# Kernel tuning notes

Hardware: AMD Instinct MI355X
Metric: run time of the kernel (lower is better)

## Reference

```python
import jax, jax.numpy as jnp
import numpy as np

B, NQ, NK, D = 8, 4096, 4096, 512


def setup_inputs() -> dict:
    key = jax.random.key(0)
    ks = jax.random.split(key, 8)
    s = 1.0 / np.sqrt(D)
    return {
        "x": jax.random.normal(ks[0], (B, NQ, D), dtype=jnp.float32),
        "context": jax.random.normal(ks[1], (B, NK, D), dtype=jnp.float32),
        "Wq": jax.random.normal(ks[2], (D, D), dtype=jnp.float32) * s,
        "bq": jax.random.normal(ks[3], (D,), dtype=jnp.float32) * 0.01,
        "Wk": jax.random.normal(ks[4], (D, D), dtype=jnp.float32) * s,
        "bk": jax.random.normal(ks[5], (D,), dtype=jnp.float32) * 0.01,
        "Wv": jax.random.normal(ks[6], (D, D), dtype=jnp.float32) * s,
        "bv": jax.random.normal(ks[7], (D,), dtype=jnp.float32) * 0.01,
    }


def reference(x, context, Wq, bq, Wk, bk, Wv, bv):
    # torch Linear: y = x @ W.T + b, W is [out, in]
    Q = jnp.einsum('bnd,ed->bne', x, Wq) + bq          # [B, NQ, D]
    K = jnp.einsum('bmd,ed->bme', context, Wk) + bk    # [B, NK, D]
    V = jnp.einsum('bmd,ed->bme', context, Wv) + bv    # [B, NK, D]
    scale = 1.0 / jnp.sqrt(jnp.asarray(x.shape[-1], dtype=x.dtype))
    scores = jnp.einsum('bne,bme->bnm', Q, K) * scale  # [B, NQ, NK]
    attn = jax.nn.softmax(scores, axis=-1)
    return jnp.einsum('bnm,bme->bne', attn, V)         # [B, NQ, D]
```

## Files before the change

### kernel.cpp

```cpp
#include <hip/hip_runtime.h>
#include <math.h>

typedef unsigned short u16;
typedef unsigned int u32;
typedef __attribute__((ext_vector_type(8))) short short8;
typedef __attribute__((ext_vector_type(4))) float floatx4;

#define DEVINL static __device__ __forceinline__

DEVINL u32 pk2(float a, float b) {
  u32 r;
  asm("v_cvt_pk_bf16_f32 %0, %1, %2" : "=v"(r) : "v"(a), "v"(b));
  return r;
}
DEVINL float exp2fast(float x) {
  float r;
  asm("v_exp_f32 %0, %1" : "=v"(r) : "v"(x));
  return r;
}

DEVINL void gload16(const void* g, void* lds_base) {
  __builtin_amdgcn_global_load_lds(
      (const __attribute__((address_space(1))) void*)g,
      (__attribute__((address_space(3))) void*)lds_base, 16, 0, 0);
}

DEVINL void stage_a_f32(const float* __restrict__ A, int lda, int gm0, int k0,
                        u16* As, int tid) {
  const int idx = tid & 127;
  const int row8 = idx >> 4;
  const int k16h = idx & 15;
  const int chsel = tid >> 7;
#pragma unroll
  for (int rr = 0; rr < 8; ++rr) {
    const int chunk = rr * 2 + chsel;
    const float4 v = *(const float4*)(A + (long)(gm0 + chunk * 8 + row8) * lda + k0 + k16h * 4);
    const int baddr = chunk * 1024 + row8 * 128 + (((k16h >> 1) ^ row8) << 4) + ((k16h & 1) << 3);
    uint2 p; p.x = pk2(v.x, v.y); p.y = pk2(v.z, v.w);
    *(uint2*)((char*)As + baddr) = p;
  }
}

__global__ __launch_bounds__(256) void cast4_kernel(const float* __restrict__ in,
                                                    u16* __restrict__ out, long n4) {
  long i = (long)blockIdx.x * blockDim.x + threadIdx.x;
  long stride = (long)gridDim.x * blockDim.x;
  for (; i < n4; i += stride) {
    float4 v = ((const float4*)in)[i];
    uint2 o; o.x = pk2(v.x, v.y); o.y = pk2(v.z, v.w);
    ((uint2*)out)[i] = o;
  }
}

__global__ __launch_bounds__(256) void zerof(float* __restrict__ p, int n4) {
  int i = blockIdx.x * 256 + threadIdx.x;
  if (i < n4) ((float4*)p)[i] = make_float4(0.f, 0.f, 0.f, 0.f);
}

__global__ __launch_bounds__(256) void proj_q(const float* __restrict__ A,
                                              const u16* __restrict__ Bt,
                                              const float* __restrict__ bias,
                                              u16* __restrict__ C, float oscale) {
  __shared__ u16 As[8192];
  __shared__ u16 Bs[8192];
  const int tid = threadIdx.x;
  const int lane = tid & 63;
  const int wave = tid >> 6;
  const int gm0 = blockIdx.y * 128;
  const int gn0 = blockIdx.x * 128;
  const int wm = (wave >> 1) * 64;
  const int wn = (wave & 1) * 64;

  floatx4 acc[4][4];
#pragma unroll
  for (int i = 0; i < 4; ++i)
#pragma unroll
    for (int j = 0; j < 4; ++j)
#pragma unroll
      for (int r = 0; r < 4; ++r) acc[i][j][r] = 0.0f;

  const int lrow = lane >> 3;
  const int lcol = (lane & 7) ^ lrow;
  const int fr_row = lane & 15;
  const int fr_k16 = lane >> 4;

  for (int k0 = 0; k0 < 512; k0 += 64) {
#pragma unroll
    for (int c = 0; c < 4; ++c) {
      const int ch = wave * 4 + c;
      gload16(Bt + (long)(gn0 + ch * 8 + lrow) * 512 + k0 + lcol * 8, (char*)Bs + ch * 1024);
    }
    stage_a_f32(A, 512, gm0, k0, As, tid);
    __syncthreads();
#pragma unroll
    for (int ks = 0; ks < 2; ++ks) {
      const int c16 = ks * 4 + fr_k16;
      short8 af[4], bfv[4];
#pragma unroll
      for (int i = 0; i < 4; ++i) {
        const int m = wm + i * 16 + fr_row;
        const int slot = (m >> 3) * 64 + (m & 7) * 8 + (c16 ^ (m & 7));
        af[i] = *(const short8*)((const char*)As + slot * 16);
      }
#pragma unroll
      for (int j = 0; j < 4; ++j) {
        const int n = wn + j * 16 + fr_row;
        const int slot = (n >> 3) * 64 + (n & 7) * 8 + (c16 ^ (n & 7));
        bfv[j] = *(const short8*)((const char*)Bs + slot * 16);
      }
#pragma unroll
      for (int i = 0; i < 4; ++i)
#pragma unroll
        for (int j = 0; j < 4; ++j)
          acc[i][j] = __builtin_amdgcn_mfma_f32_16x16x32_bf16(af[i], bfv[j], acc[i][j], 0, 0, 0);
    }
    __syncthreads();
  }

  const int crow = (lane >> 4) * 4;
  const int ccol = lane & 15;
#pragma unroll
  for (int i = 0; i < 4; ++i)
#pragma unroll
    for (int j = 0; j < 4; ++j) {
      const int n = gn0 + wn + j * 16 + ccol;
      const float badd = bias[n];
      const float a0 = (acc[i][j][0] + badd) * oscale;
      const float a1 = (acc[i][j][1] + badd) * oscale;
      const float a2 = (acc[i][j][2] + badd) * oscale;
      const float a3 = (acc[i][j][3] + badd) * oscale;
      const u32 p01 = pk2(a0, a1);
      const u32 p23 = pk2(a2, a3);
      u16* cp = C + (long)(gm0 + wm + i * 16 + crow) * 512 + n;
      cp[0]    = (u16)p01;
      cp[512]  = (u16)(p01 >> 16);
      cp[1024] = (u16)p23;
      cp[1536] = (u16)(p23 >> 16);
    }
}

__global__ __launch_bounds__(256) void proj_kv(const float* __restrict__ A,
                                               const u16* __restrict__ Wk,
                                               const float* __restrict__ bk,
                                               const u16* __restrict__ Wv,
                                               const float* __restrict__ bv,
                                               u16* __restrict__ Kb,
                                               u16* __restrict__ Vt) {
  __shared__ u16 As[8192];
  __shared__ u16 Bs[8192];
  const int tid = threadIdx.x;
  const int lane = tid & 63;
  const int wave = tid >> 6;
  const int isV = blockIdx.x >> 2;
  const u16* Bt = isV ? Wv : Wk;
  const float* bias = isV ? bv : bk;
  const int gm0 = blockIdx.y * 128;
  const int gn0 = (blockIdx.x & 3) * 128;
  const int wm = (wave >> 1) * 64;
  const int wn = (wave & 1) * 64;

  floatx4 acc[4][4];
#pragma unroll
  for (int i = 0; i < 4; ++i)
#pragma unroll
    for (int j = 0; j < 4; ++j)
#pragma unroll
      for (int r = 0; r < 4; ++r) acc[i][j][r] = 0.0f;

  const int lrow = lane >> 3;
  const int lcol = (lane & 7) ^ lrow;
  const int fr_row = lane & 15;
  const int fr_k16 = lane >> 4;

  for (int k0 = 0; k0 < 512; k0 += 64) {
#pragma unroll
    for (int c = 0; c < 4; ++c) {
      const int ch = wave * 4 + c;
      gload16(Bt + (long)(gn0 + ch * 8 + lrow) * 512 + k0 + lcol * 8, (char*)Bs + ch * 1024);
    }
    stage_a_f32(A, 512, gm0, k0, As, tid);
    __syncthreads();
#pragma unroll
    for (int ks = 0; ks < 2; ++ks) {
      const int c16 = ks * 4 + fr_k16;
      short8 af[4], bfv[4];
#pragma unroll
      for (int i = 0; i < 4; ++i) {
        const int m = wm + i * 16 + fr_row;
        const int slot = (m >> 3) * 64 + (m & 7) * 8 + (c16 ^ (m & 7));
        af[i] = *(const short8*)((const char*)As + slot * 16);
      }
#pragma unroll
      for (int j = 0; j < 4; ++j) {
        const int n = wn + j * 16 + fr_row;
        const int slot = (n >> 3) * 64 + (n & 7) * 8 + (c16 ^ (n & 7));
        bfv[j] = *(const short8*)((const char*)Bs + slot * 16);
      }
#pragma unroll
      for (int i = 0; i < 4; ++i)
#pragma unroll
        for (int j = 0; j < 4; ++j)
          acc[i][j] = __builtin_amdgcn_mfma_f32_16x16x32_bf16(af[i], bfv[j], acc[i][j], 0, 0, 0);
    }
    __syncthreads();
  }

  const int crow = (lane >> 4) * 4;
  const int ccol = lane & 15;
  if (!isV) {
#pragma unroll
    for (int i = 0; i < 4; ++i)
#pragma unroll
      for (int j = 0; j < 4; ++j) {
        const int n = gn0 + wn + j * 16 + ccol;
        const float badd = bias[n];
        const u32 p01 = pk2(acc[i][j][0] + badd, acc[i][j][1] + badd);
        const u32 p23 = pk2(acc[i][j][2] + badd, acc[i][j][3] + badd);
        u16* cp = Kb + (long)(gm0 + wm + i * 16 + crow) * 512 + n;
        cp[0]    = (u16)p01;
        cp[512]  = (u16)(p01 >> 16);
        cp[1024] = (u16)p23;
        cp[1536] = (u16)(p23 >> 16);
      }
  } else {
#pragma unroll
    for (int i = 0; i < 4; ++i)
#pragma unroll
      for (int j = 0; j < 4; ++j) {
        const int n = gn0 + wn + j * 16 + ccol;
        const float badd = bias[n];
        const int m = gm0 + wm + i * 16 + crow;
        const int b = m >> 12;
        const int mm = m & 4095;
        uint2 st;
        st.x = pk2(acc[i][j][0] + badd, acc[i][j][1] + badd);
        st.y = pk2(acc[i][j][2] + badd, acc[i][j][3] + badd);
        *(uint2*)(Vt + (long)b * 512 * 4096 + (long)n * 4096 + mm) = st;
      }
  }
}

__global__ __launch_bounds__(256) void gemm_s(
    const u16* __restrict__ A, const u16* __restrict__ Bt, u16* __restrict__ S,
    float* __restrict__ Ld, long aBS, long bBS) {
  __shared__ u16 As[8192];
  __shared__ u16 Bs[8192];
  const int tid = threadIdx.x;
  const int lane = tid & 63;
  const int wave = tid >> 6;
  const int bz = blockIdx.z;
  A += (long)bz * aBS;
  Bt += (long)bz * bBS;
  u16* Sb = S + (long)bz * 4096 * 4096;
  const int gm0 = blockIdx.y * 128;
  const int gn0 = blockIdx.x * 128;
  const int wm = (wave >> 1) * 64;
  const int wn = (wave & 1) * 64;

  floatx4 acc[4][4];
#pragma unroll
  for (int i = 0; i < 4; ++i)
#pragma unroll
    for (int j = 0; j < 4; ++j)
#pragma unroll
      for (int r = 0; r < 4; ++r) acc[i][j][r] = 0.0f;

  const int lrow = lane >> 3;
  const int lcol = (lane & 7) ^ lrow;
  const int fr_row = lane & 15;
  const int fr_k16 = lane >> 4;

  for (int k0 = 0; k0 < 512; k0 += 64) {
#pragma unroll
    for (int c = 0; c < 4; ++c) {
      const int ch = wave * 4 + c;
      const int r = ch * 8 + lrow;
      gload16(A + (long)(gm0 + r) * 512 + k0 + lcol * 8, (char*)As + ch * 1024);
      gload16(Bt + (long)(gn0 + r) * 512 + k0 + lcol * 8, (char*)Bs + ch * 1024);
    }
    __syncthreads();
#pragma unroll
    for (int ks = 0; ks < 2; ++ks) {
      const int c16 = ks * 4 + fr_k16;
      short8 af[4], bfv[4];
#pragma unroll
      for (int i = 0; i < 4; ++i) {
        const int m = wm + i * 16 + fr_row;
        const int slot = (m >> 3) * 64 + (m & 7) * 8 + (c16 ^ (m & 7));
        af[i] = *(const short8*)((const char*)As + slot * 16);
      }
#pragma unroll
      for (int j = 0; j < 4; ++j) {
        const int n = wn + j * 16 + fr_row;
        const int slot = (n >> 3) * 64 + (n & 7) * 8 + (c16 ^ (n & 7));
        bfv[j] = *(const short8*)((const char*)Bs + slot * 16);
      }
#pragma unroll
      for (int i = 0; i < 4; ++i)
#pragma unroll
        for (int j = 0; j < 4; ++j)
          acc[i][j] = __builtin_amdgcn_mfma_f32_16x16x32_bf16(af[i], bfv[j], acc[i][j], 0, 0, 0);
    }
    __syncthreads();
  }

  const int crow = (lane >> 4) * 4;
  const int ccol = lane & 15;
  float (*sml)[2] = (float (*)[2])As;
#pragma unroll
  for (int i = 0; i < 4; ++i) {
    float rs0 = 0.f, rs1 = 0.f, rs2 = 0.f, rs3 = 0.f;
    u16* sp = Sb + (long)(gm0 + wm + i * 16 + crow) * 4096 + gn0 + wn + ccol;
#pragma unroll
    for (int j = 0; j < 4; ++j) {
      const float e0 = exp2fast(acc[i][j][0]);
      const float e1 = exp2fast(acc[i][j][1]);
      const float e2 = exp2fast(acc[i][j][2]);
      const float e3 = exp2fast(acc[i][j][3]);
      const u32 p01 = pk2(e0, e1);
      const u32 p23 = pk2(e2, e3);
      u16* q = sp + j * 16;
      q[0]     = (u16)p01;
      q[4096]  = (u16)(p01 >> 16);
      q[8192]  = (u16)p23;
      q[12288] = (u16)(p23 >> 16);
      rs0 += e0; rs1 += e1; rs2 += e2; rs3 += e3;
    }
#pragma unroll
    for (int off = 1; off < 16; off <<= 1) {
      rs0 += __shfl_xor(rs0, off, 64);
      rs1 += __shfl_xor(rs1, off, 64);
      rs2 += __shfl_xor(rs2, off, 64);
      rs3 += __shfl_xor(rs3, off, 64);
    }
    if ((lane & 15) == 0) {
      const int rb = wm + i * 16 + crow;
      sml[rb + 0][wave & 1] = rs0;
      sml[rb + 1][wave & 1] = rs1;
      sml[rb + 2][wave & 1] = rs2;
      sml[rb + 3][wave & 1] = rs3;
    }
  }
  __syncthreads();
  if (tid < 128)
    atomicAdd(&Ld[(long)bz * 4096 + gm0 + tid], sml[tid][0] + sml[tid][1]);
}

__global__ __launch_bounds__(256) void gemm_o(
    const u16* __restrict__ A, const u16* __restrict__ Bt, float* __restrict__ Cout,
    const float* __restrict__ Ld, long aBS, long bBS, long cBS) {
  __shared__ u16 As[4096];
  __shared__ u16 Bs[8192];
  const int tid = threadIdx.x;
  const int lane = tid & 63;
  const int wave = tid >> 6;
  const int bz = blockIdx.z;
  A += (long)bz * aBS;
  Bt += (long)bz * bBS;
  const long cbase = (long)bz * cBS;
  const int gm0 = blockIdx.y * 64;
  const int gn0 = blockIdx.x * 128;
  const int wn = wave * 32;

  floatx4 acc[4][2];
#pragma unroll
  for (int i = 0; i < 4; ++i)
#pragma unroll
    for (int j = 0; j < 2; ++j)
#pragma unroll
      for (int r = 0; r < 4; ++r) acc[i][j][r] = 0.0f;

  const int lrow = lane >> 3;
  const int lcol = (lane & 7) ^ lrow;
  const int fr_row = lane & 15;
  const int fr_k16 = lane >> 4;

  for (int k0 = 0; k0 < 4096; k0 += 64) {
#pragma unroll
    for (int c = 0; c < 2; ++c) {
      const int ch = wave * 2 + c;
      gload16(A + (long)(gm0 + ch * 8 + lrow) * 4096 + k0 + lcol * 8, (char*)As + ch * 1024);
    }
#pragma unroll
    for (int c = 0; c < 4; ++c) {
      const int ch = wave * 4 + c;
      gload16(Bt + (long)(gn0 + ch * 8 + lrow) * 4096 + k0 + lcol * 8, (char*)Bs + ch * 1024);
    }
    __syncthreads();
#pragma unroll
    for (int ks = 0; ks < 2; ++ks) {
      const int c16 = ks * 4 + fr_k16;
      short8 af[4], bfv[2];
#pragma unroll
      for (int i = 0; i < 4; ++i) {
        const int m = i * 16 + fr_row;
        const int slot = (m >> 3) * 64 + (m & 7) * 8 + (c16 ^ (m & 7));
        af[i] = *(const short8*)((const char*)As + slot * 16);
      }
#pragma unroll
      for (int j = 0; j < 2; ++j) {
        const int n = wn + j * 16 + fr_row;
        const int slot = (n >> 3) * 64 + (n & 7) * 8 + (c16 ^ (n & 7));
        bfv[j] = *(const short8*)((const char*)Bs + slot * 16);
      }
#pragma unroll
      for (int i = 0; i < 4; ++i)
#pragma unroll
        for (int j = 0; j < 2; ++j)
          acc[i][j] = __builtin_amdgcn_mfma_f32_16x16x32_bf16(af[i], bfv[j], acc[i][j], 0, 0, 0);
    }
    __syncthreads();
  }

  const int crow = (lane >> 4) * 4;
  const int ccol = lane & 15;
  float linv[4][4];
#pragma unroll
  for (int i = 0; i < 4; ++i)
#pragma unroll
    for (int r = 0; r < 4; ++r)
      linv[i][r] = 1.0f / Ld[(long)bz * 4096 + gm0 + i * 16 + crow + r];
#pragma unroll
  for (int i = 0; i < 4; ++i)
#pragma unroll
    for (int j = 0; j < 2; ++j) {
      const int n = gn0 + wn + j * 16 + ccol;
#pragma unroll
      for (int r = 0; r < 4; ++r) {
        const int m = gm0 + i * 16 + crow + r;
        Cout[cbase + (long)m * 512 + n] = acc[i][j][r] * linv[i][r];
      }
    }
}

extern "C" void kernel_launch(void* const* d_in, const int* in_sizes, int n_in,
                              void* d_out, int out_size, void* d_ws, size_t ws_size,
                              hipStream_t stream) {
  const int B = 8, NQ = 4096, NK = 4096, D = 512;
  const long nX = (long)B * NQ * D;
  const long nW = (long)D * D;
  const float oscale = 0.044194173824159216f * 1.4426950408889634f;

  const float* x = (const float*)d_in[0];
  const float* ctx = (const float*)d_in[1];
  const float* Wq = (const float*)d_in[2];
  const float* bq = (const float*)d_in[3];
  const float* Wk = (const float*)d_in[4];
  const float* bk = (const float*)d_in[5];
  const float* Wv = (const float*)d_in[6];
  const float* bv = (const float*)d_in[7];
  float* out = (float*)d_out;

  size_t off = 0;
  auto alloc = [&](size_t bytes) { size_t o = off; off = (off + bytes + 255) & ~(size_t)255; return o; };
  char* ws = (char*)d_ws;
  u16* Qb  = (u16*)(ws + alloc(nX * 2));
  u16* Kb  = (u16*)(ws + alloc(nX * 2));
  u16* Vt  = (u16*)(ws + alloc(nX * 2));
  float* Ld = (float*)(ws + alloc((size_t)B * NQ * 4));
  const size_t s_off = off;
  u16* wqb = (u16*)(ws + alloc(nW * 2));
  u16* wkb = (u16*)(ws + alloc(nW * 2));
  u16* wvb = (u16*)(ws + alloc(nW * 2));
  u16* S   = (u16*)(ws + s_off);

  const size_t sBatch = (size_t)NQ * NK * 2;
  const size_t avail = (ws_size > s_off) ? (ws_size - s_off) : 0;
  int nb = (int)(avail / sBatch);
  if (nb > 8) nb = 8;
  else if (nb >= 4 && nb < 8) nb = 4;
  if (nb < 1) nb = 1;

  cast4_kernel<<<128, 256, 0, stream>>>(Wq, wqb, nW / 4);
  cast4_kernel<<<128, 256, 0, stream>>>(Wk, wkb, nW / 4);
  cast4_kernel<<<128, 256, 0, stream>>>(Wv, wvb, nW / 4);
  zerof<<<(B * NQ / 4 + 255) / 256, 256, 0, stream>>>(Ld, B * NQ / 4);

  proj_q<<<dim3(4, 256), 256, 0, stream>>>(x, wqb, bq, Qb, oscale);
  proj_kv<<<dim3(8, 256), 256, 0, stream>>>(ctx, wkb, bk, wvb, bv, Kb, Vt);

  for (int b0 = 0; b0 < B; b0 += nb) {
    const int nbb = (b0 + nb <= B) ? nb : (B - b0);
    gemm_s<<<dim3(32, 32, nbb), 256, 0, stream>>>(
        Qb + (long)b0 * NQ * D, Kb + (long)b0 * NK * D, S,
        Ld + (long)b0 * NQ, (long)NQ * D, (long)NK * D);
    gemm_o<<<dim3(4, 64, nbb), 256, 0, stream>>>(
        S, Vt + (long)b0 * D * NK, out + (long)b0 * NQ * D,
        Ld + (long)b0 * NQ, (long)NQ * NK, (long)D * NK, (long)NQ * D);
  }
  (void)in_sizes; (void)n_in; (void)out_size;
}
```

Baseline: 745.8 us.

## Load MFMA fragments directly from global memory in score GEMM and swizzle tile order

The score GEMM no longer stages A and B tiles through LDS with barriers. Each wave now loads its MFMA fragments straight from global memory, relying on L1/L2 caching for reuse across waves. The block index is also remapped so that consecutive blocks share A/B rows, which should improve L2 hit rate. This removes LDS traffic and synchronisation but duplicates global loads across waves and exposes more memory latency.

```diff
diff --git a/kernel.cpp b/kernel.cpp
--- a/kernel.cpp
+++ b/kernel.cpp
@@ -243,8 +243,7 @@
 __global__ __launch_bounds__(256) void gemm_s(
     const u16* __restrict__ A, const u16* __restrict__ Bt, u16* __restrict__ S,
     float* __restrict__ Ld, long aBS, long bBS) {
-  __shared__ u16 As[8192];
-  __shared__ u16 Bs[8192];
+  __shared__ float sml[128][2];
   const int tid = threadIdx.x;
   const int lane = tid & 63;
   const int wave = tid >> 6;
@@ -252,8 +251,10 @@
   A += (long)bz * aBS;
   Bt += (long)bz * bBS;
   u16* Sb = S + (long)bz * 4096 * 4096;
-  const int gm0 = blockIdx.y * 128;
-  const int gn0 = blockIdx.x * 128;
+  const int bid = blockIdx.y * 32 + blockIdx.x;
+  const int swz = (bid & 7) * 128 + (bid >> 3);
+  const int gm0 = (swz >> 5) * 128;
+  const int gn0 = (swz & 31) * 128;
   const int wm = (wave >> 1) * 64;
   const int wn = (wave & 1) * 64;
 
@@ -265,48 +266,37 @@
 #pragma unroll
       for (int r = 0; r < 4; ++r) acc[i][j][r] = 0.0f;
 
-  const int lrow = lane >> 3;
-  const int lcol = (lane & 7) ^ lrow;
   const int fr_row = lane & 15;
   const int fr_k16 = lane >> 4;
-
-  for (int k0 = 0; k0 < 512; k0 += 64) {
-#pragma unroll
-    for (int c = 0; c < 4; ++c) {
-      const int ch = wave * 4 + c;
-      const int r = ch * 8 + lrow;
-      gload16(A + (long)(gm0 + r) * 512 + k0 + lcol * 8, (char*)As + ch * 1024);
-      gload16(Bt + (long)(gn0 + r) * 512 + k0 + lcol * 8, (char*)Bs + ch * 1024);
-    }
-    __syncthreads();
-#pragma unroll
-    for (int ks = 0; ks < 2; ++ks) {
-      const int c16 = ks * 4 + fr_k16;
-      short8 af[4], bfv[4];
-#pragma unroll
-      for (int i = 0; i < 4; ++i) {
-        const int m = wm + i * 16 + fr_row;
-        const int slot = (m >> 3) * 64 + (m & 7) * 8 + (c16 ^ (m & 7));
-        af[i] = *(const short8*)((const char*)As + slot * 16);
-      }
-#pragma unroll
-      for (int j = 0; j < 4; ++j) {
-        const int n = wn + j * 16 + fr_row;
-        const int slot = (n >> 3) * 64 + (n & 7) * 8 + (c16 ^ (n & 7));
-        bfv[j] = *(const short8*)((const char*)Bs + slot * 16);
-      }
-#pragma unroll
-      for (int i = 0; i < 4; ++i)
-#pragma unroll
-        for (int j = 0; j < 4; ++j)
-          acc[i][j] = __builtin_amdgcn_mfma_f32_16x16x32_bf16(af[i], bfv[j], acc[i][j], 0, 0, 0);
-    }
-    __syncthreads();
+  const u16* a0 = A + (long)(gm0 + wm + fr_row) * 512 + fr_k16 * 8;
+  const u16* a1 = a0 + 16 * 512;
+  const u16* a2 = a0 + 32 * 512;
+  const u16* a3 = a0 + 48 * 512;
+  const u16* b0 = Bt + (long)(gn0 + wn + fr_row) * 512 + fr_k16 * 8;
+  const u16* b1 = b0 + 16 * 512;
+  const u16* b2 = b0 + 32 * 512;
+  const u16* b3 = b0 + 48 * 512;
+
+#pragma unroll 2
+  for (int kc = 0; kc < 16; ++kc) {
+    short8 af[4], bfv[4];
+    af[0]  = *(const short8*)(a0 + kc * 32);
+    af[1]  = *(const short8*)(a1 + kc * 32);
+    af[2]  = *(const short8*)(a2 + kc * 32);
+    af[3]  = *(const short8*)(a3 + kc * 32);
+    bfv[0] = *(const short8*)(b0 + kc * 32);
+    bfv[1] = *(const short8*)(b1 + kc * 32);
+    bfv[2] = *(const short8*)(b2 + kc * 32);
+    bfv[3] = *(const short8*)(b3 + kc * 32);
+#pragma unroll
+    for (int i = 0; i < 4; ++i)
+#pragma unroll
+      for (int j = 0; j < 4; ++j)
+        acc[i][j] = __builtin_amdgcn_mfma_f32_16x16x32_bf16(af[i], bfv[j], acc[i][j], 0, 0, 0);
   }
 
   const int crow = (lane >> 4) * 4;
   const int ccol = lane & 15;
-  float (*sml)[2] = (float (*)[2])As;
 #pragma unroll
   for (int i = 0; i < 4; ++i) {
     float rs0 = 0.f, rs1 = 0.f, rs2 = 0.f, rs3 = 0.f;
```

Result: slower. 983.2 us (+31.8%).

## Double-buffer LDS tiles in score and output GEMMs to overlap loads with MFMA

Applied to the files above, without the earlier changes.

Both the S=QK^T GEMM and the P·V GEMM now keep two LDS buffers and prefetch the next K-tile with direct-to-LDS global loads while the current tile is consumed. Explicit vmcnt waits plus raw s_barrier calls replace the two __syncthreads per iteration, so global memory latency is meant to hide behind MFMA work. LDS use per block doubles, which may lower occupancy, and correctness depends on the hand-counted vmcnt values matching the number of loads issued per stage.

```diff
diff --git a/kernel.cpp b/kernel.cpp
--- a/kernel.cpp
+++ b/kernel.cpp
@@ -243,8 +243,8 @@
 __global__ __launch_bounds__(256) void gemm_s(
     const u16* __restrict__ A, const u16* __restrict__ Bt, u16* __restrict__ S,
     float* __restrict__ Ld, long aBS, long bBS) {
-  __shared__ u16 As[8192];
-  __shared__ u16 Bs[8192];
+  __shared__ u16 As[2][8192];
+  __shared__ u16 Bs[2][8192];
   const int tid = threadIdx.x;
   const int lane = tid & 63;
   const int wave = tid >> 6;
@@ -270,15 +270,29 @@
   const int fr_row = lane & 15;
   const int fr_k16 = lane >> 4;
 
-  for (int k0 = 0; k0 < 512; k0 += 64) {
+  auto stage = [&](int buf, int k0) {
 #pragma unroll
     for (int c = 0; c < 4; ++c) {
       const int ch = wave * 4 + c;
       const int r = ch * 8 + lrow;
-      gload16(A + (long)(gm0 + r) * 512 + k0 + lcol * 8, (char*)As + ch * 1024);
-      gload16(Bt + (long)(gn0 + r) * 512 + k0 + lcol * 8, (char*)Bs + ch * 1024);
-    }
-    __syncthreads();
+      gload16(A + (long)(gm0 + r) * 512 + k0 + lcol * 8, (char*)As[buf] + ch * 1024);
+      gload16(Bt + (long)(gn0 + r) * 512 + k0 + lcol * 8, (char*)Bs[buf] + ch * 1024);
+    }
+  };
+
+  stage(0, 0);
+#pragma unroll 2
+  for (int kt = 0; kt < 8; ++kt) {
+    if (kt < 7) {
+      stage((kt + 1) & 1, (kt + 1) * 64);
+      asm volatile("s_waitcnt vmcnt(8)" ::: "memory");
+    } else {
+      asm volatile("s_waitcnt vmcnt(0)" ::: "memory");
+    }
+    __builtin_amdgcn_s_barrier();
+    __builtin_amdgcn_sched_barrier(0);
+    const u16* Ab = As[kt & 1];
+    const u16* Bb = Bs[kt & 1];
 #pragma unroll
     for (int ks = 0; ks < 2; ++ks) {
       const int c16 = ks * 4 + fr_k16;
@@ -287,13 +301,13 @@
       for (int i = 0; i < 4; ++i) {
         const int m = wm + i * 16 + fr_row;
         const int slot = (m >> 3) * 64 + (m & 7) * 8 + (c16 ^ (m & 7));
-        af[i] = *(const short8*)((const char*)As + slot * 16);
+        af[i] = *(const short8*)((const char*)Ab + slot * 16);
       }
 #pragma unroll
       for (int j = 0; j < 4; ++j) {
         const int n = wn + j * 16 + fr_row;
         const int slot = (n >> 3) * 64 + (n & 7) * 8 + (c16 ^ (n & 7));
-        bfv[j] = *(const short8*)((const char*)Bs + slot * 16);
+        bfv[j] = *(const short8*)((const char*)Bb + slot * 16);
       }
 #pragma unroll
       for (int i = 0; i < 4; ++i)
@@ -301,12 +315,14 @@
         for (int j = 0; j < 4; ++j)
           acc[i][j] = __builtin_amdgcn_mfma_f32_16x16x32_bf16(af[i], bfv[j], acc[i][j], 0, 0, 0);
     }
-    __syncthreads();
+    asm volatile("s_waitcnt lgkmcnt(0)" ::: "memory");
+    __builtin_amdgcn_sched_barrier(0);
+    __builtin_amdgcn_s_barrier();
   }
 
   const int crow = (lane >> 4) * 4;
   const int ccol = lane & 15;
-  float (*sml)[2] = (float (*)[2])As;
+  float (*sml)[2] = (float (*)[2])(&As[0][0]);
 #pragma unroll
   for (int i = 0; i < 4; ++i) {
     float rs0 = 0.f, rs1 = 0.f, rs2 = 0.f, rs3 = 0.f;
@@ -349,8 +365,8 @@
 __global__ __launch_bounds__(256) void gemm_o(
     const u16* __restrict__ A, const u16* __restrict__ Bt, float* __restrict__ Cout,
     const float* __restrict__ Ld, long aBS, long bBS, long cBS) {
-  __shared__ u16 As[4096];
-  __shared__ u16 Bs[8192];
+  __shared__ u16 As[2][4096];
+  __shared__ u16 Bs[2][8192];
   const int tid = threadIdx.x;
   const int lane = tid & 63;
   const int wave = tid >> 6;
@@ -375,18 +391,31 @@
   const int fr_row = lane & 15;
   const int fr_k16 = lane >> 4;
 
-  for (int k0 = 0; k0 < 4096; k0 += 64) {
+  auto stage = [&](int buf, int k0) {
 #pragma unroll
     for (int c = 0; c < 2; ++c) {
       const int ch = wave * 2 + c;
-      gload16(A + (long)(gm0 + ch * 8 + lrow) * 4096 + k0 + lcol * 8, (char*)As + ch * 1024);
+      gload16(A + (long)(gm0 + ch * 8 + lrow) * 4096 + k0 + lcol * 8, (char*)As[buf] + ch * 1024);
     }
 #pragma unroll
     for (int c = 0; c < 4; ++c) {
       const int ch = wave * 4 + c;
-      gload16(Bt + (long)(gn0 + ch * 8 + lrow) * 4096 + k0 + lcol * 8, (char*)Bs + ch * 1024);
-    }
-    __syncthreads();
+      gload16(Bt + (long)(gn0 + ch * 8 + lrow) * 4096 + k0 + lcol * 8, (char*)Bs[buf] + ch * 1024);
+    }
+  };
+
+  stage(0, 0);
+  for (int kt = 0; kt < 64; ++kt) {
+    if (kt < 63) {
+      stage((kt + 1) & 1, (kt + 1) * 64);
+      asm volatile("s_waitcnt vmcnt(6)" ::: "memory");
+    } else {
+      asm volatile("s_waitcnt vmcnt(0)" ::: "memory");
+    }
+    __builtin_amdgcn_s_barrier();
+    __builtin_amdgcn_sched_barrier(0);
+    const u16* Ab = As[kt & 1];
+    const u16* Bb = Bs[kt & 1];
 #pragma unroll
     for (int ks = 0; ks < 2; ++ks) {
       const int c16 = ks * 4 + fr_k16;
@@ -395,13 +424,13 @@
       for (int i = 0; i < 4; ++i) {
         const int m = i * 16 + fr_row;
         const int slot = (m >> 3) * 64 + (m & 7) * 8 + (c16 ^ (m & 7));
-        af[i] = *(const short8*)((const char*)As + slot * 16);
+        af[i] = *(const short8*)((const char*)Ab + slot * 16);
       }
 #pragma unroll
       for (int j = 0; j < 2; ++j) {
         const int n = wn + j * 16 + fr_row;
         const int slot = (n >> 3) * 64 + (n & 7) * 8 + (c16 ^ (n & 7));
-        bfv[j] = *(const short8*)((const char*)Bs + slot * 16);
+        bfv[j] = *(const short8*)((const char*)Bb + slot * 16);
       }
 #pragma unroll
       for (int i = 0; i < 4; ++i)
@@ -409,7 +438,9 @@
         for (int j = 0; j < 2; ++j)
           acc[i][j] = __builtin_amdgcn_mfma_f32_16x16x32_bf16(af[i], bfv[j], acc[i][j], 0, 0, 0);
     }
-    __syncthreads();
+    asm volatile("s_waitcnt lgkmcnt(0)" ::: "memory");
+    __builtin_amdgcn_sched_barrier(0);
+    __builtin_amdgcn_s_barrier();
   }
 
   const int crow = (lane >> 4) * 4;
```

Result: slower. 834.8 us (+11.9%).
